# Performance work log

Measured on AMD Instinct MI355X. Metric: run time of the kernel, lower is better.

Reference implementation:

```python
import jax, jax.numpy as jnp
import numpy as np

WS = 7        # window size (cubic)
SHIFT = 3     # shift size (cubic)
NH = 6        # num heads
EPS = 1e-5


def _layernorm(x, g, b):
    m = x.mean(-1, keepdims=True)
    v = ((x - m) ** 2).mean(-1, keepdims=True)
    return (x - m) / jnp.sqrt(v + EPS) * g + b


def _win_partition(x, ws):
    # (B,H,W,T,C) -> (B*nW, ws^3, C)
    B, H, W, T, C = x.shape
    x = x.reshape(B, H // ws, ws, W // ws, ws, T // ws, ws, C)
    return x.transpose(0, 1, 3, 5, 2, 4, 6, 7).reshape(-1, ws * ws * ws, C)


def _win_reverse(w, ws, B, H, W, T):
    # (B*nW, ws^3, C) -> (B,H,W,T,C)
    C = w.shape[-1]
    x = w.reshape(B, H // ws, W // ws, T // ws, ws, ws, ws, C)
    return x.transpose(0, 1, 4, 2, 5, 3, 6, 7).reshape(B, H, W, T, C)


def _rel_index(ws):
    # 3D relative position index, (N, N) int, N = ws^3 (torch.meshgrid default 'ij')
    coords = np.stack(np.meshgrid(np.arange(ws), np.arange(ws), np.arange(ws), indexing='ij'))
    cf = coords.reshape(3, -1)
    rel = (cf[:, :, None] - cf[:, None, :]).transpose(1, 2, 0)
    rel[:, :, 0] += ws - 1
    rel[:, :, 1] += ws - 1
    rel[:, :, 2] += ws - 1
    rel[:, :, 0] *= (2 * ws - 1) ** 2
    rel[:, :, 1] *= (2 * ws - 1)
    return rel.sum(-1)


def _compute_mask(Hp, Wp, Tp, ws, shift):
    img = np.zeros((1, Hp, Wp, Tp, 1), np.float32)
    cnt = 0
    sl = (slice(0, -ws), slice(-ws, -shift), slice(-shift, None))
    for h in sl:
        for w in sl:
            for t in sl:
                img[:, h, w, t, :] = cnt
                cnt += 1
    mw = np.asarray(_win_partition(jnp.asarray(img), ws)).reshape(-1, ws ** 3)  # (nW, N)
    am = mw[:, None, :] - mw[:, :, None]
    return jnp.asarray(np.where(am != 0, -100.0, 0.0).astype(np.float32))


def setup_inputs() -> dict:
    key = jax.random.key(0)
    ks = jax.random.split(key, 10)
    B, Hd, Wd, Td, C = 2, 28, 28, 28, 192
    L = Hd * Wd * Td
    Ch = int(C * 4.0)
    s = 0.02
    inp = {
        'x': jax.random.normal(ks[0], (B, L, C), jnp.float32),
        'mask': _compute_mask(Hd, Wd, Td, WS, SHIFT),
        'gamma1': jnp.ones((C,), jnp.float32),
        'beta1': jnp.zeros((C,), jnp.float32),
        'qkv_w': jax.random.normal(ks[1], (3 * C, C), jnp.float32) * s,
        'qkv_b': jnp.zeros((3 * C,), jnp.float32),
        'rpb_table': jax.random.normal(ks[2], ((2 * WS - 1) ** 3, NH), jnp.float32) * s,
        'proj_w': jax.random.normal(ks[3], (C, C), jnp.float32) * s,
        'proj_b': jnp.zeros((C,), jnp.float32),
        'gamma2': jnp.ones((C,), jnp.float32),
        'beta2': jnp.zeros((C,), jnp.float32),
        'fc1_w': jax.random.normal(ks[4], (Ch, C), jnp.float32) * s,
        'fc1_b': jnp.zeros((Ch,), jnp.float32),
        'fc2_w': jax.random.normal(ks[5], (C, Ch), jnp.float32) * s,
        'fc2_b': jnp.zeros((C,), jnp.float32),
        'H': Hd, 'W': Wd, 'T': Td,
    }
    return inp


def reference(x, mask, gamma1, beta1, qkv_w, qkv_b, rpb_table, proj_w, proj_b,
              gamma2, beta2, fc1_w, fc1_b, fc2_w, fc2_b, H, W, T):
    B, L, C = x.shape
    hd = C // NH
    scale = hd ** -0.5
    shortcut = x

    h1 = _layernorm(x, gamma1, beta1).reshape(B, H, W, T, C)
    # H,W,T are multiples of WS -> no padding; cyclic shift for SW-MSA
    shifted = jnp.roll(h1, (-SHIFT, -SHIFT, -SHIFT), axis=(1, 2, 3))
    xw = _win_partition(shifted, WS)            # (B*nW, N, C)
    Bn, N, _ = xw.shape

    qkv = (xw @ qkv_w.T + qkv_b).reshape(Bn, N, 3, NH, hd).transpose(2, 0, 3, 1, 4)
    q, k, v = qkv[0] * scale, qkv[1], qkv[2]     # (Bn, NH, N, hd)
    attn = jnp.einsum('bhnd,bhmd->bhnm', q, k)   # (Bn, NH, N, N)

    idx = _rel_index(WS)
    bias = rpb_table[idx.reshape(-1)].reshape(N, N, NH).transpose(2, 0, 1)
    attn = attn + bias[None]

    nW = mask.shape[0]
    attn = attn.reshape(Bn // nW, nW, NH, N, N) + mask[None, :, None]
    attn = jax.nn.softmax(attn.reshape(Bn, NH, N, N), axis=-1)

    out = jnp.einsum('bhnm,bhmd->bhnd', attn, v).transpose(0, 2, 1, 3).reshape(Bn, N, C)
    out = out @ proj_w.T + proj_b

    shifted = _win_reverse(out, WS, B, H, W, T)
    xr = jnp.roll(shifted, (SHIFT, SHIFT, SHIFT), axis=(1, 2, 3)).reshape(B, L, C)

    x = shortcut + xr
    h2 = _layernorm(x, gamma2, beta2)
    m = jax.nn.gelu(h2 @ fc1_w.T + fc1_b, approximate=False)
    return x + (m @ fc2_w.T + fc2_b)
```

## Files before the change

### kernel.cpp

```cpp
#include <hip/hip_runtime.h>
#include <hip/hip_bf16.h>

typedef unsigned short u16;
typedef unsigned int u32;
typedef __attribute__((ext_vector_type(8))) short s16x8;
typedef __attribute__((ext_vector_type(4))) float f32x4;

__device__ __forceinline__ float bf2f(u16 v) {
    union { u32 u; float f; } x; x.u = ((u32)v) << 16; return x.f;
}
__device__ __forceinline__ u16 f2bf(float f) {
    union { float f; u32 u; } x; x.f = f;
    u32 r = x.u + 0x7fffu + ((x.u >> 16) & 1u);
    return (u16)(r >> 16);
}
__device__ __forceinline__ u32 cvt_pk_bf16(float a, float b) {
    u32 r;
    asm("v_cvt_pk_bf16_f32 %0, %1, %2" : "=v"(r) : "v"(a), "v"(b));
    return r;
}
__device__ __forceinline__ void gl2lds(const u16* g, u16* l) {
    __builtin_amdgcn_global_load_lds(
        (const __attribute__((address_space(1))) unsigned int*)g,
        (__attribute__((address_space(3))) unsigned int*)l, 16, 0, 0);
}

#define L_TOK 21952
#define C_DIM 192
#define LOG2E 1.4426950408889634f
#define Q2SCALE 0.2550565444463649f
#define BF_STR 352

__global__ __launch_bounds__(256) void cvt_k(const float* __restrict__ s0,
                                             const float* __restrict__ s1,
                                             const float* __restrict__ s2,
                                             const float* __restrict__ s3,
                                             u16* __restrict__ dst)
{
    int i = blockIdx.x * 256 + threadIdx.x;
    float v;
    if (i < 110592) v = s0[i];
    else if (i < 147456) v = s1[i - 110592];
    else if (i < 294912) v = s2[i - 147456];
    else v = s3[i - 294912];
    dst[i] = f2bf(v);
}

__global__ __launch_bounds__(256) void bias48_k(const float* __restrict__ rpb,
                                                float* __restrict__ biasF)
{
    const int gid = blockIdx.x * 256 + threadIdx.x;
    const int z = gid / 30976;
    const int rem = gid - z * 30976;
    const int m = rem / 88;
    const int n0 = (rem - m * 88) * 4;
    const int hh = z >> 3, wt = z & 7;

    f32x4 vout;
    if (m <= 342) {
        const int hm = m / 49, r2 = m - hm * 49, wm = r2 / 7, tm = r2 - wm * 7;
        const int rm = ((wt & 4) ? (hm < 4 ? 1 : 2) : 0) * 9
                     + ((wt & 2) ? (wm < 4 ? 1 : 2) : 0) * 3
                     + ((wt & 1) ? (tm < 4 ? 1 : 2) : 0);
        #pragma unroll
        for (int j = 0; j < 4; j++) {
            const int n = n0 + j;
            float v = -100000.0f;
            if (n <= 342) {
                int hq = n / 49, r1 = n - hq * 49, wq = r1 / 7, tq = r1 - wq * 7;
                int idx = ((hq - hm + 6) * 13 + (wq - wm + 6)) * 13 + (tq - tm + 6);
                float b = rpb[idx * 6 + hh];
                int rq = ((wt & 4) ? (hq < 4 ? 1 : 2) : 0) * 9
                       + ((wt & 2) ? (wq < 4 ? 1 : 2) : 0) * 3
                       + ((wt & 1) ? (tq < 4 ? 1 : 2) : 0);
                if (rq != rm) b -= 100.0f;
                v = b * LOG2E;
            }
            vout[j] = v;
        }
    } else {
        vout = (f32x4){-100000.0f, -100000.0f, -100000.0f, -100000.0f};
    }
    *(f32x4*)&biasF[((size_t)z * 352 + m) * BF_STR + n0] = vout;
}

template<int MODE>
__global__ __launch_bounds__(256) void ln_k(const float* __restrict__ in,
                                            const float* __restrict__ g,
                                            const float* __restrict__ b,
                                            u16* __restrict__ out)
{
    const int lane = threadIdx.x & 63, wv = threadIdx.x >> 6;
    const int tok = blockIdx.x * 4 + wv;
    size_t base = (size_t)tok * C_DIM;
    float x0 = in[base + lane];
    float x1 = in[base + 64 + lane];
    float x2 = in[base + 128 + lane];
    float s = x0 + x1 + x2;
    float sq = x0 * x0 + x1 * x1 + x2 * x2;
    #pragma unroll
    for (int off = 32; off > 0; off >>= 1) {
        s += __shfl_xor(s, off, 64);
        sq += __shfl_xor(sq, off, 64);
    }
    const float mean = s * (1.0f / 192.0f);
    float var = sq * (1.0f / 192.0f) - mean * mean;
    var = fmaxf(var, 0.0f);
    const float rstd = rsqrtf(var + 1e-5f);

    size_t obase;
    if (MODE == 0) {
        int bi = tok / L_TOK;
        int l = tok - bi * L_TOK;
        int h = l / 784;
        int rm = l - h * 784;
        int w = rm / 28;
        int t = rm - w * 28;
        int hs = h + 25; if (hs >= 28) hs -= 28;
        int ws = w + 25; if (ws >= 28) ws -= 28;
        int ts = t + 25; if (ts >= 28) ts -= 28;
        int win = ((bi * 4 + hs / 7) * 4 + ws / 7) * 4 + ts / 7;
        int n = (hs % 7) * 49 + (ws % 7) * 7 + (ts % 7);
        obase = ((size_t)win * 343 + n) * C_DIM;
    } else {
        obase = base;
    }
    #pragma unroll
    for (int i = 0; i < 3; i++) {
        int c = lane + i * 64;
        float xv = (i == 0) ? x0 : (i == 1) ? x1 : x2;
        float y = (xv - mean) * rstd * g[c] + b[c];
        out[obase + c] = f2bf(y);
    }
}

template<int K, int EPI>
__global__ __launch_bounds__(256) void gemm_k(const u16* __restrict__ A,
                                              const u16* __restrict__ W,
                                              const float* __restrict__ bias,
                                              void* __restrict__ outp,
                                              const void* __restrict__ resp,
                                              int Ncols)
{
    __shared__ __align__(16) u16 As[3 * 128 * 32];
    __shared__ __align__(16) u16 Bs[3 * 64 * 32];
    const int t = threadIdx.x;
    const int bm = blockIdx.y;
    const int n0 = blockIdx.x * 64;
    const int lane = t & 63, wv = t >> 6;
    const int wm = (wv >> 1) * 64, wn = (wv & 1) * 32;
    const int r16 = lane & 15, quad = lane >> 4;

    f32x4 acc[4][2];
    #pragma unroll
    for (int i = 0; i < 4; i++)
        #pragma unroll
        for (int j = 0; j < 2; j++) acc[i][j] = (f32x4){0.f, 0.f, 0.f, 0.f};

    const int ar = t >> 2, ac = (t & 3) * 8;
    const size_t abase = (size_t)bm * 128 * K;

    for (int kc = 0; kc < K; kc += 96) {
        if (kc) __syncthreads();
        #pragma unroll
        for (int kt = 0; kt < 3; kt++) {
            const int k0 = kc + kt * 32;
            gl2lds(&A[abase + (size_t)ar * K + k0 + ac], &As[kt * 4096 + 8 * t]);
            gl2lds(&A[abase + (size_t)(ar + 64) * K + k0 + ac], &As[kt * 4096 + 2048 + 8 * t]);
            gl2lds(&W[(size_t)(n0 + ar) * K + k0 + ac], &Bs[kt * 2048 + 8 * t]);
        }
        __syncthreads();
        #pragma unroll
        for (int kt = 0; kt < 3; kt++) {
            s16x8 af[4], bf[2];
            #pragma unroll
            for (int fm = 0; fm < 4; fm++)
                af[fm] = *(const s16x8*)&As[kt * 4096 + (wm + fm * 16 + r16) * 32 + quad * 8];
            #pragma unroll
            for (int fn = 0; fn < 2; fn++)
                bf[fn] = *(const s16x8*)&Bs[kt * 2048 + (wn + fn * 16 + r16) * 32 + quad * 8];
            #pragma unroll
            for (int fm = 0; fm < 4; fm++)
                #pragma unroll
                for (int fn = 0; fn < 2; fn++)
                    acc[fm][fn] = __builtin_amdgcn_mfma_f32_16x16x32_bf16(af[fm], bf[fn], acc[fm][fn], 0, 0, 0);
        }
    }

    #pragma unroll
    for (int fm = 0; fm < 4; fm++) {
        #pragma unroll
        for (int fn = 0; fn < 2; fn++) {
            #pragma unroll
            for (int r = 0; r < 4; r++) {
                const int grow = bm * 128 + wm + fm * 16 + quad * 4 + r;
                const int gcol = n0 + wn + fn * 16 + r16;
                float v = acc[fm][fn][r] + bias[gcol];
                if (EPI == 0) {
                    if (gcol < 192) v *= Q2SCALE;
                    ((u16*)outp)[(size_t)grow * Ncols + gcol] = f2bf(v);
                } else if (EPI == 1) {
                    v = 0.5f * v * (1.0f + erff(v * 0.70710678118654752f));
                    ((u16*)outp)[(size_t)grow * Ncols + gcol] = f2bf(v);
                } else if (EPI == 2) {
                    size_t o = (size_t)grow * C_DIM + gcol;
                    ((float*)outp)[o] = v + ((const float*)resp)[o];
                } else {
                    int win = grow / 343, n = grow - win * 343;
                    int bi = win >> 6, wi = win & 63;
                    int hw = wi >> 4, ww = (wi >> 2) & 3, tw = wi & 3;
                    int ph = n / 49, rem = n - ph * 49;
                    int pw = rem / 7, pt = rem - pw * 7;
                    int h = hw * 7 + ph + 3; if (h >= 28) h -= 28;
                    int w = ww * 7 + pw + 3; if (w >= 28) w -= 28;
                    int tt = tw * 7 + pt + 3; if (tt >= 28) tt -= 28;
                    int l = (h * 28 + w) * 28 + tt;
                    size_t o = ((size_t)bi * L_TOK + l) * C_DIM + gcol;
                    ((float*)outp)[o] = v + ((const float*)resp)[o];
                }
            }
        }
    }
}

__global__ __launch_bounds__(256, 3) void attn_k(const u16* __restrict__ qkv,
                                                 const float* __restrict__ biasAll,
                                                 u16* __restrict__ out)
{
    __shared__ __align__(16) u16 Ks[352 * 32];
    __shared__ __align__(16) u16 Vt[32 * 360];
    __shared__ __align__(16) u16 Pb[4][16 * 40];

    const int hh = blockIdx.x;
    const int win = blockIdx.y;
    const int wi = win & 63;
    const int t = threadIdx.x, lane = t & 63, wv = t >> 6;
    const int r16 = lane & 15, quad = lane >> 4;
    const size_t qbase = (size_t)win * 343 * 576 + hh * 32;

    for (int j = t; j < 343 * 4; j += 256) {
        int m = j >> 2, ch = j & 3;
        *(uint4*)&Ks[m * 32 + ch * 8] = *(const uint4*)&qkv[qbase + (size_t)m * 576 + 192 + ch * 8];
    }
    if (t < 36) {
        int m = 343 + (t >> 2), ch = t & 3;
        *(uint4*)&Ks[m * 32 + ch * 8] = (uint4){0u, 0u, 0u, 0u};
    }
    for (int i = t; i < 343 * 16; i += 256) {
        int m = i >> 4, d2 = (i & 15) * 2;
        int pm = (m & ~31) + 2 * (m & 15) + ((m >> 4) & 1);
        u32 w2 = *(const u32*)&qkv[qbase + (size_t)m * 576 + 384 + d2];
        Vt[d2 * 360 + pm] = (u16)(w2 & 0xffffu);
        Vt[(d2 + 1) * 360 + pm] = (u16)(w2 >> 16);
    }
    for (int i = t; i < 32 * 9; i += 256) {
        int d = i / 9, m = 343 + i % 9;
        int pm = (m & ~31) + 2 * (m & 15) + ((m >> 4) & 1);
        Vt[d * 360 + pm] = 0;
    }
    __syncthreads();

    const int wt = (((wi >> 4) == 3) ? 4 : 0) | ((((wi >> 2) & 3) == 3) ? 2 : 0)
                 | (((wi & 3) == 3) ? 1 : 0);
    const float* biashT = biasAll + (size_t)(hh * 8 + wt) * 352 * BF_STR;

    s16x8 onesb;
    #pragma unroll
    for (int j = 0; j < 8; j++) onesb[j] = (short)0x3f80;

    for (int qt = 0; qt < 6; qt++) {
        const int row0 = qt * 64 + wv * 16;
        if (row0 > 342) continue;
        int qrow = row0 + r16; if (qrow > 342) qrow = 342;
        s16x8 qa = *(const s16x8*)&qkv[qbase + (size_t)qrow * 576 + quad * 8];

        const int n0 = row0 + quad * 4;

        f32x4 sacc[22];
        #pragma unroll
        for (int fn = 0; fn < 22; fn++) {
            const int col = fn * 16 + r16;
            sacc[fn] = *(const f32x4*)&biashT[(size_t)col * BF_STR + n0];
        }
        #pragma unroll
        for (int fn = 0; fn < 22; fn++) {
            s16x8 kb = *(const s16x8*)&Ks[(fn * 16 + r16) * 32 + quad * 8];
            sacc[fn] = __builtin_amdgcn_mfma_f32_16x16x32_bf16(qa, kb, sacc[fn], 0, 0, 0);
        }

        #pragma unroll
        for (int fn = 0; fn < 22; fn++) {
            #pragma unroll
            for (int r = 0; r < 4; r++)
                sacc[fn][r] = exp2f(fminf(sacc[fn][r], 42.0f));
        }

        u16* pw = &Pb[wv][0];
        u32* pw32 = (u32*)pw;
        f32x4 oacc0 = (f32x4){0.f, 0.f, 0.f, 0.f};
        f32x4 oacc1 = (f32x4){0.f, 0.f, 0.f, 0.f};
        f32x4 osum  = (f32x4){0.f, 0.f, 0.f, 0.f};
        #pragma unroll
        for (int c = 0; c < 11; c++) {
            asm volatile("s_waitcnt lgkmcnt(0)" ::: "memory");
            #pragma unroll
            for (int r = 0; r < 4; r++)
                pw32[(quad * 4 + r) * 20 + r16] = cvt_pk_bf16(sacc[2 * c][r], sacc[2 * c + 1][r]);
            asm volatile("s_waitcnt lgkmcnt(0)" ::: "memory");
            s16x8 pa = *(const s16x8*)&pw[r16 * 40 + quad * 8];
            s16x8 vb0 = *(const s16x8*)&Vt[r16 * 360 + c * 32 + quad * 8];
            s16x8 vb1 = *(const s16x8*)&Vt[(16 + r16) * 360 + c * 32 + quad * 8];
            oacc0 = __builtin_amdgcn_mfma_f32_16x16x32_bf16(pa, vb0, oacc0, 0, 0, 0);
            oacc1 = __builtin_amdgcn_mfma_f32_16x16x32_bf16(pa, vb1, oacc1, 0, 0, 0);
            osum  = __builtin_amdgcn_mfma_f32_16x16x32_bf16(pa, onesb, osum, 0, 0, 0);
        }

        #pragma unroll
        for (int r = 0; r < 4; r++) {
            const int n = n0 + r;
            if (n < 343) {
                const float rs = osum[r];
                const float inv = rs > 0.0f ? 1.0f / rs : 0.0f;
                size_t o = ((size_t)win * 343 + n) * C_DIM + hh * 32;
                out[o + r16] = f2bf(oacc0[r] * inv);
                out[o + 16 + r16] = f2bf(oacc1[r] * inv);
            }
        }
    }
}

extern "C" void kernel_launch(void* const* d_in, const int* in_sizes, int n_in,
                              void* d_out, int out_size, void* d_ws, size_t ws_size,
                              hipStream_t stream)
{
    const float* x      = (const float*)d_in[0];
    const float* g1     = (const float*)d_in[2];
    const float* b1     = (const float*)d_in[3];
    const float* qkv_w  = (const float*)d_in[4];
    const float* qkv_b  = (const float*)d_in[5];
    const float* rpb    = (const float*)d_in[6];
    const float* proj_w = (const float*)d_in[7];
    const float* proj_b = (const float*)d_in[8];
    const float* g2     = (const float*)d_in[9];
    const float* b2     = (const float*)d_in[10];
    const float* fc1_w  = (const float*)d_in[11];
    const float* fc1_b  = (const float*)d_in[12];
    const float* fc2_w  = (const float*)d_in[13];
    const float* fc2_b  = (const float*)d_in[14];

    char* ws = (char*)d_ws;
    u16* xw        = (u16*)(ws + 0);
    u16* qkv       = (u16*)(ws + 16861184);
    u16* a1        = (u16*)(ws + 0);
    u16* attn_out  = (u16*)(ws + 67444736);
    u16* h2        = attn_out;
    float* x2      = (float*)(ws + 84305920);
    float* biasF   = x2;
    u16* wbf       = (u16*)(ws + 118028288);
    u16* qkv_wb = wbf;
    u16* proj_wb = wbf + 110592;
    u16* fc1_wb = wbf + 147456;
    u16* fc2_wb = wbf + 294912;

    cvt_k<<<dim3(1728), 256, 0, stream>>>(qkv_w, proj_w, fc1_w, fc2_w, wbf);
    ln_k<0><<<dim3(10976), 256, 0, stream>>>(x, g1, b1, xw);
    gemm_k<192, 0><<<dim3(9, 343), 256, 0, stream>>>(xw, qkv_wb, qkv_b, qkv, nullptr, 576);
    bias48_k<<<dim3(5808), 256, 0, stream>>>(rpb, biasF);
    attn_k<<<dim3(6, 128), 256, 0, stream>>>(qkv, biasF, attn_out);
    gemm_k<192, 3><<<dim3(3, 343), 256, 0, stream>>>(attn_out, proj_wb, proj_b, x2, x, 192);
    ln_k<1><<<dim3(10976), 256, 0, stream>>>(x2, g2, b2, h2);
    gemm_k<192, 1><<<dim3(12, 343), 256, 0, stream>>>(h2, fc1_wb, fc1_b, a1, nullptr, 768);
    gemm_k<768, 2><<<dim3(3, 343), 256, 0, stream>>>(a1, fc2_wb, fc2_b, d_out, x2, 192);
}
```

Before: 358.1 us.

## Store relative-position bias as per-head bf16 and apply shift mask in-kernel

The precomputed bias table shrinks from 48 fp32 variants (head × window type, with the shift mask folded in) to 6 bf16 per-head tables. The attention kernel now builds per-token region ids in shared memory and zeroes exp values whose query and key regions differ, so the bias the kernel reads per score tile is much smaller. Two explicit LDS waitcnt barriers in the PV loop are also removed. The trade-offs are bf16 rounding of the bias, extra compare and select work for boundary windows, and relying on the compiler to order the shared-memory write and read of P correctly.

```diff
diff --git a/kernel.cpp b/kernel.cpp
--- a/kernel.cpp
+++ b/kernel.cpp
@@ -6,14 +6,17 @@
 typedef __attribute__((ext_vector_type(8))) short s16x8;
 typedef __attribute__((ext_vector_type(4))) float f32x4;
 
-__device__ __forceinline__ float bf2f(u16 v) {
-    union { u32 u; float f; } x; x.u = ((u32)v) << 16; return x.f;
-}
 __device__ __forceinline__ u16 f2bf(float f) {
     union { float f; u32 u; } x; x.f = f;
     u32 r = x.u + 0x7fffu + ((x.u >> 16) & 1u);
     return (u16)(r >> 16);
 }
+__device__ __forceinline__ float bflo(u32 v) {
+    union { u32 u; float f; } x; x.u = v << 16; return x.f;
+}
+__device__ __forceinline__ float bfhi(u32 v) {
+    union { u32 u; float f; } x; x.u = v & 0xffff0000u; return x.f;
+}
 __device__ __forceinline__ u32 cvt_pk_bf16(float a, float b) {
     u32 r;
     asm("v_cvt_pk_bf16_f32 %0, %1, %2" : "=v"(r) : "v"(a), "v"(b));
@@ -29,7 +32,6 @@
 #define C_DIM 192
 #define LOG2E 1.4426950408889634f
 #define Q2SCALE 0.2550565444463649f
-#define BF_STR 352
 
 __global__ __launch_bounds__(256) void cvt_k(const float* __restrict__ s0,
                                              const float* __restrict__ s1,
@@ -46,42 +48,36 @@
     dst[i] = f2bf(v);
 }
 
-__global__ __launch_bounds__(256) void bias48_k(const float* __restrict__ rpb,
-                                                float* __restrict__ biasF)
+__global__ __launch_bounds__(256) void bias6_k(const float* __restrict__ rpb,
+                                               u16* __restrict__ biasT)
 {
     const int gid = blockIdx.x * 256 + threadIdx.x;
-    const int z = gid / 30976;
-    const int rem = gid - z * 30976;
+    const int hh = gid / 30976;
+    const int rem = gid - hh * 30976;
     const int m = rem / 88;
     const int n0 = (rem - m * 88) * 4;
-    const int hh = z >> 3, wt = z & 7;
-
-    f32x4 vout;
+
+    u16 v[4];
     if (m <= 342) {
         const int hm = m / 49, r2 = m - hm * 49, wm = r2 / 7, tm = r2 - wm * 7;
-        const int rm = ((wt & 4) ? (hm < 4 ? 1 : 2) : 0) * 9
-                     + ((wt & 2) ? (wm < 4 ? 1 : 2) : 0) * 3
-                     + ((wt & 1) ? (tm < 4 ? 1 : 2) : 0);
         #pragma unroll
         for (int j = 0; j < 4; j++) {
             const int n = n0 + j;
-            float v = -100000.0f;
+            float b = -100000.0f;
             if (n <= 342) {
                 int hq = n / 49, r1 = n - hq * 49, wq = r1 / 7, tq = r1 - wq * 7;
                 int idx = ((hq - hm + 6) * 13 + (wq - wm + 6)) * 13 + (tq - tm + 6);
-                float b = rpb[idx * 6 + hh];
-                int rq = ((wt & 4) ? (hq < 4 ? 1 : 2) : 0) * 9
-                       + ((wt & 2) ? (wq < 4 ? 1 : 2) : 0) * 3
-                       + ((wt & 1) ? (tq < 4 ? 1 : 2) : 0);
-                if (rq != rm) b -= 100.0f;
-                v = b * LOG2E;
+                b = rpb[idx * 6 + hh] * LOG2E;
             }
-            vout[j] = v;
+            v[j] = f2bf(b);
         }
     } else {
-        vout = (f32x4){-100000.0f, -100000.0f, -100000.0f, -100000.0f};
-    }
-    *(f32x4*)&biasF[((size_t)z * 352 + m) * BF_STR + n0] = vout;
+        const u16 neg = f2bf(-100000.0f);
+        v[0] = neg; v[1] = neg; v[2] = neg; v[3] = neg;
+    }
+    u32 lo = (u32)v[0] | ((u32)v[1] << 16);
+    u32 hi = (u32)v[2] | ((u32)v[3] << 16);
+    *(uint2*)&biasT[((size_t)hh * 352 + m) * 352 + n0] = (uint2){lo, hi};
 }
 
 template<int MODE>
@@ -224,12 +220,13 @@
 }
 
 __global__ __launch_bounds__(256, 3) void attn_k(const u16* __restrict__ qkv,
-                                                 const float* __restrict__ biasAll,
+                                                 const u16* __restrict__ biasAll,
                                                  u16* __restrict__ out)
 {
     __shared__ __align__(16) u16 Ks[352 * 32];
     __shared__ __align__(16) u16 Vt[32 * 360];
     __shared__ __align__(16) u16 Pb[4][16 * 40];
+    __shared__ u16 Cn[352];
 
     const int hh = blockIdx.x;
     const int win = blockIdx.y;
@@ -258,11 +255,31 @@
         int pm = (m & ~31) + 2 * (m & 15) + ((m >> 4) & 1);
         Vt[d * 360 + pm] = 0;
     }
+    const int hw = (wi >> 4) & 3, ww = (wi >> 2) & 3, tw = wi & 3;
+    const int wt = (hw == 3 ? 4 : 0) | (ww == 3 ? 2 : 0) | (tw == 3 ? 1 : 0);
+    if (wt) {
+        for (int n = t; n < 352; n += 256) {
+            int nn = n > 342 ? 342 : n;
+            int ph = nn / 49, rem = nn - ph * 49;
+            int pw = rem / 7, pt = rem - pw * 7;
+            int rh = (hw == 3) ? (ph < 4 ? 1 : 2) : 0;
+            int rw = (ww == 3) ? (pw < 4 ? 1 : 2) : 0;
+            int rt = (tw == 3) ? (pt < 4 ? 1 : 2) : 0;
+            Cn[n] = (u16)(rh * 9 + rw * 3 + rt);
+        }
+    }
     __syncthreads();
 
-    const int wt = (((wi >> 4) == 3) ? 4 : 0) | ((((wi >> 2) & 3) == 3) ? 2 : 0)
-                 | (((wi & 3) == 3) ? 1 : 0);
-    const float* biashT = biasAll + (size_t)(hh * 8 + wt) * 352 * BF_STR;
+    const u16* biashT = biasAll + (size_t)hh * 352 * 352;
+
+    u16 cntc[22];
+    if (wt) {
+        #pragma unroll
+        for (int fn = 0; fn < 22; fn++) {
+            int col = fn * 16 + r16; if (col > 342) col = 342;
+            cntc[fn] = Cn[col];
+        }
+    }
 
     s16x8 onesb;
     #pragma unroll
@@ -280,7 +297,11 @@
         #pragma unroll
         for (int fn = 0; fn < 22; fn++) {
             const int col = fn * 16 + r16;
-            sacc[fn] = *(const f32x4*)&biashT[(size_t)col * BF_STR + n0];
+            uint2 bv = *(const uint2*)&biashT[(size_t)col * 352 + n0];
+            sacc[fn][0] = bflo(bv.x);
+            sacc[fn][1] = bfhi(bv.x);
+            sacc[fn][2] = bflo(bv.y);
+            sacc[fn][3] = bfhi(bv.y);
         }
         #pragma unroll
         for (int fn = 0; fn < 22; fn++) {
@@ -288,11 +309,27 @@
             sacc[fn] = __builtin_amdgcn_mfma_f32_16x16x32_bf16(qa, kb, sacc[fn], 0, 0, 0);
         }
 
-        #pragma unroll
-        for (int fn = 0; fn < 22; fn++) {
-            #pragma unroll
-            for (int r = 0; r < 4; r++)
-                sacc[fn][r] = exp2f(fminf(sacc[fn][r], 42.0f));
+        if (wt == 0) {
+            #pragma unroll
+            for (int fn = 0; fn < 22; fn++)
+                #pragma unroll
+                for (int r = 0; r < 4; r++)
+                    sacc[fn][r] = exp2f(fminf(sacc[fn][r], 42.0f));
+        } else {
+            u16 cr[4];
+            #pragma unroll
+            for (int r = 0; r < 4; r++) {
+                int n = n0 + r; if (n > 342) n = 342;
+                cr[r] = Cn[n];
+            }
+            #pragma unroll
+            for (int fn = 0; fn < 22; fn++) {
+                #pragma unroll
+                for (int r = 0; r < 4; r++) {
+                    float p = exp2f(fminf(sacc[fn][r], 42.0f));
+                    sacc[fn][r] = (cntc[fn] == cr[r]) ? p : 0.0f;
+                }
+            }
         }
 
         u16* pw = &Pb[wv][0];
@@ -302,11 +339,9 @@
         f32x4 osum  = (f32x4){0.f, 0.f, 0.f, 0.f};
         #pragma unroll
         for (int c = 0; c < 11; c++) {
-            asm volatile("s_waitcnt lgkmcnt(0)" ::: "memory");
             #pragma unroll
             for (int r = 0; r < 4; r++)
                 pw32[(quad * 4 + r) * 20 + r16] = cvt_pk_bf16(sacc[2 * c][r], sacc[2 * c + 1][r]);
-            asm volatile("s_waitcnt lgkmcnt(0)" ::: "memory");
             s16x8 pa = *(const s16x8*)&pw[r16 * 40 + quad * 8];
             s16x8 vb0 = *(const s16x8*)&Vt[r16 * 360 + c * 32 + quad * 8];
             s16x8 vb1 = *(const s16x8*)&Vt[(16 + r16) * 360 + c * 32 + quad * 8];
@@ -350,12 +385,12 @@
 
     char* ws = (char*)d_ws;
     u16* xw        = (u16*)(ws + 0);
+    u16* biasT     = (u16*)(ws + 0);
     u16* qkv       = (u16*)(ws + 16861184);
     u16* a1        = (u16*)(ws + 0);
     u16* attn_out  = (u16*)(ws + 67444736);
     u16* h2        = attn_out;
     float* x2      = (float*)(ws + 84305920);
-    float* biasF   = x2;
     u16* wbf       = (u16*)(ws + 118028288);
     u16* qkv_wb = wbf;
     u16* proj_wb = wbf + 110592;
@@ -365,8 +400,8 @@
     cvt_k<<<dim3(1728), 256, 0, stream>>>(qkv_w, proj_w, fc1_w, fc2_w, wbf);
     ln_k<0><<<dim3(10976), 256, 0, stream>>>(x, g1, b1, xw);
     gemm_k<192, 0><<<dim3(9, 343), 256, 0, stream>>>(xw, qkv_wb, qkv_b, qkv, nullptr, 576);
-    bias48_k<<<dim3(5808), 256, 0, stream>>>(rpb, biasF);
-    attn_k<<<dim3(6, 128), 256, 0, stream>>>(qkv, biasF, attn_out);
+    bias6_k<<<dim3(726), 256, 0, stream>>>(rpb, biasT);
+    attn_k<<<dim3(6, 128), 256, 0, stream>>>(qkv, biasT, attn_out);
     gemm_k<192, 3><<<dim3(3, 343), 256, 0, stream>>>(attn_out, proj_wb, proj_b, x2, x, 192);
     ln_k<1><<<dim3(10976), 256, 0, stream>>>(x2, g2, b2, h2);
     gemm_k<192, 1><<<dim3(12, 343), 256, 0, stream>>>(h2, fc1_wb, fc1_b, a1, nullptr, 768);
```

Measured after the change: 402.0 us. 1.12x slower.
